# Kernel tuning notes

Measured on AMD Instinct MI355X. Metric: run time of the kernel, lower is better.

The kernel has to match this reference:

```python
import jax, jax.numpy as jnp
import numpy as np

B, HH, WW, DV, DC = 4, 128, 128, 768, 128
INNER = 2 * DV          # inner_ratio * values_dim = 1536
NH = 8                  # num_heads
DH = INNER // NH        # 192
SPACING = 4
COORDS_WEIGHT = 1.0     # attention_coords_weight
EPS = 1e-6


def _anchor_idx(h, w, s, shifted=False):
    rows = np.arange(0, h, s)
    cols = np.arange(0, w, s)
    if not shifted:
        rows = rows + ((h - 1) % s) // 2
        cols = cols + ((w - 1) % s) // 2
    return rows, cols


def _rms(x, w):
    return x * jax.lax.rsqrt(jnp.mean(x * x, axis=-1, keepdims=True) + EPS) * w


def _heads(x):  # (b, n, h*d) -> (b, h, n, d)
    b, n, _ = x.shape
    return x.reshape(b, n, NH, DH).transpose(0, 2, 1, 3)


def setup_inputs() -> dict:
    key = jax.random.key(0)
    ks = jax.random.split(key, 12)
    inp = {
        "values0": jax.random.normal(ks[0], (B, HH, WW, DV), jnp.float32),
        "coords0": jax.random.normal(ks[1], (B, HH, WW, DC), jnp.float32),
        "values1": jax.random.normal(ks[2], (B, HH, WW, DV), jnp.float32),
        "coords1": jax.random.normal(ks[3], (B, HH, WW, DC), jnp.float32),
        # values_to_qkv: Linear(DV, 3*INNER, bias=False), stored as (in, out)
        "w_qkv": jax.random.normal(ks[4], (DV, 3 * INNER), jnp.float32) * (DV ** -0.5),
        "qnorm_w": jnp.ones((INNER,), jnp.float32),
        "knorm_w": jnp.ones((INNER,), jnp.float32),
        # coords_to_qk: Linear(DC, 2*INNER, bias=False) + RMSNorm(2*INNER)
        "w_coords": jax.random.normal(ks[5], (DC, 2 * INNER), jnp.float32) * (DC ** -0.5),
        "coords_norm_w": jnp.ones((2 * INNER,), jnp.float32),
        "rel_pos_weight": jax.random.normal(ks[6], (1,), jnp.float32),
        # output_proj: Linear(INNER, DV)
        "out_w": jax.random.normal(ks[7], (INNER, DV), jnp.float32) * (INNER ** -0.5),
        "out_b": jnp.zeros((DV,), jnp.float32),
    }
    return inp


def reference(values0, coords0, values1, coords1, w_qkv, qnorm_w, knorm_w,
              w_coords, coords_norm_w, rel_pos_weight, out_w, out_b):
    rows, cols = _anchor_idx(HH, WW, SPACING)
    na = len(rows) * len(cols)  # anchors per source (1024)

    def gather(x):  # (B, HH, WW, D) -> (B, na, D)
        return x[:, rows[:, None], cols].reshape(B, na, -1)

    av = jnp.concatenate([gather(values0), gather(values1)], axis=1)  # (B, 2na, DV)
    ac = jnp.concatenate([gather(coords0), gather(coords1)], axis=1)  # (B, 2na, DC)

    qv, kv, vv = jnp.split(av @ w_qkv, 3, axis=-1)
    qv = _rms(qv, qnorm_w)
    kv = _rms(kv, knorm_w)
    qc, kc = jnp.split(_rms(ac @ w_coords, coords_norm_w), 2, axis=-1)

    qv, kv, vv, qc, kc = map(_heads, (qv, kv, vv, qc, kc))  # (B, NH, N, DH)

    scale = DH ** -0.5
    dots = jnp.einsum('bhqd,bhkd->bhqk', qv, kv) * scale
    rel = jnp.einsum('bhqd,bhkd->bhqk', qc, kc) * scale
    dots = dots + (rel_pos_weight[0] * COORDS_WEIGHT) * rel
    attn = jax.nn.softmax(dots, axis=-1)

    out = jnp.einsum('bhqk,bhkd->bhqd', attn, vv)          # (B, NH, N, DH)
    out = out.transpose(0, 2, 1, 3).reshape(B, 2 * na, INNER)
    out = out @ out_w + out_b                               # (B, 2na, DV)

    a0 = out[:, :na].reshape(B, len(rows), len(cols), DV)
    a1 = out[:, na:].reshape(B, len(rows), len(cols), DV)

    o0 = values0.at[:, rows[:, None], cols, :].add(a0)
    o1 = values1.at[:, rows[:, None], cols, :].add(a1)
    return jnp.stack([o0, o1])  # (2, B, HH, WW, DV)
```

## Files before the change

kernel.cpp:

```cpp
#include <hip/hip_runtime.h>

typedef unsigned short u16;
typedef unsigned int u32;
typedef float f32x4 __attribute__((ext_vector_type(4)));
typedef short bfx8 __attribute__((ext_vector_type(8)));
typedef u16 u16x8 __attribute__((ext_vector_type(8)));
typedef u16 u16x4 __attribute__((ext_vector_type(4)));

#define MFMA_BF16(a,b,c) __builtin_amdgcn_mfma_f32_16x16x32_bf16((a),(b),(c),0,0,0)
#define GL16(src, dst) __builtin_amdgcn_global_load_lds( \
    (const __attribute__((address_space(1))) u32*)(src), \
    (__attribute__((address_space(3))) u32*)(dst), 16, 0, 0)

__device__ __forceinline__ u16 f2bf(float f) {
  unsigned u = __float_as_uint(f);
  u += 0x7fffu + ((u >> 16) & 1u);
  return (u16)(u >> 16);
}
__device__ __forceinline__ float bf2f(u16 h) {
  return __uint_as_float((unsigned)h << 16);
}

#define SCALE_ATTN 0.07216878364870323f

__global__ __launch_bounds__(256) void wtrans_kernel(
    const float* __restrict__ in, u16* __restrict__ out, int K, int N)
{
  __shared__ float tile[32][33];
  int n0 = blockIdx.x * 32, k0 = blockIdx.y * 32;
  int tx = threadIdx.x, ty = threadIdx.y;
#pragma unroll
  for (int j = 0; j < 32; j += 8)
    tile[ty + j][tx] = in[(size_t)(k0 + ty + j) * N + n0 + tx];
  __syncthreads();
#pragma unroll
  for (int j = 0; j < 32; j += 8)
    out[(size_t)(n0 + ty + j) * K + k0 + tx] = f2bf(tile[tx][ty + j]);
}

__global__ __launch_bounds__(256) void gather_kernel(
    const float* __restrict__ v0, const float* __restrict__ c0,
    const float* __restrict__ v1, const float* __restrict__ c1,
    u16* __restrict__ av, u16* __restrict__ ac)
{
  int t = blockIdx.x;
  int b = t >> 11, n = t & 2047, s = n >> 10, a = n & 1023, rr = a >> 5, cc = a & 31;
  size_t pix = ((size_t)b * 128 + (1 + 4 * rr)) * 128 + (1 + 4 * cc);
  const float4* vs = (const float4*)((s ? v1 : v0) + pix * 768);
  const float4* cs = (const float4*)((s ? c1 : c0) + pix * 128);
  int tid = threadIdx.x;
  if (tid < 192) {
    float4 f = vs[tid];
    u16x4 o = { f2bf(f.x), f2bf(f.y), f2bf(f.z), f2bf(f.w) };
    *(u16x4*)(av + (size_t)t * 768 + tid * 4) = o;
  }
  if (tid < 32) {
    float4 f = cs[tid];
    u16x4 o = { f2bf(f.x), f2bf(f.y), f2bf(f.z), f2bf(f.w) };
    *(u16x4*)(ac + (size_t)t * 128 + tid * 4) = o;
  }
}

template<int EPILOG>
__global__ __launch_bounds__(256) void gemm128(
    const u16* __restrict__ A, const u16* __restrict__ Bt,
    int K, int lda, int ldb,
    u16* __restrict__ qp, u16* __restrict__ kp, u16* __restrict__ vT,
    float* __restrict__ outAdd, const float* __restrict__ bias)
{
  __shared__ u16 As[128 * 32];
  __shared__ u16 Bs[128 * 32];
  const int tid = threadIdx.x;
  const int wid = tid >> 6, lane = tid & 63;
  const int g = lane >> 4, q15 = lane & 15;
  const int wm = wid >> 1, wn = wid & 1;
  const int m0 = blockIdx.y * 128, n0 = blockIdx.x * 128;

  const u16* ga = A + (size_t)(m0 + (tid >> 2)) * lda + (tid & 3) * 8;
  const u16* gb = Bt + (size_t)(n0 + (tid >> 2)) * ldb + (tid & 3) * 8;
  u16* lA0 = &As[tid * 8]; u16* lA1 = &As[2048 + tid * 8];
  u16* lB0 = &Bs[tid * 8]; u16* lB1 = &Bs[2048 + tid * 8];
  const size_t a64 = (size_t)64 * lda, b64 = (size_t)64 * ldb;

  const f32x4 zero = {0.f, 0.f, 0.f, 0.f};
  f32x4 acc[4][4];
#pragma unroll
  for (int i = 0; i < 4; i++)
#pragma unroll
    for (int j = 0; j < 4; j++) acc[i][j] = zero;

  for (int kk = 0; kk < K; kk += 32) {
    GL16(ga + kk, lA0);
    GL16(ga + kk + a64, lA1);
    GL16(gb + kk, lB0);
    GL16(gb + kk + b64, lB1);
    __syncthreads();
    bfx8 af[4], bf[4];
#pragma unroll
    for (int mt = 0; mt < 4; mt++)
      af[mt] = *(const bfx8*)&As[(wm * 64 + mt * 16 + q15) * 32 + g * 8];
#pragma unroll
    for (int nt = 0; nt < 4; nt++)
      bf[nt] = *(const bfx8*)&Bs[(wn * 64 + nt * 16 + q15) * 32 + g * 8];
#pragma unroll
    for (int mt = 0; mt < 4; mt++)
#pragma unroll
      for (int nt = 0; nt < 4; nt++)
        acc[mt][nt] = MFMA_BF16(af[mt], bf[nt], acc[mt][nt]);
    __syncthreads();
  }

#pragma unroll
  for (int mt = 0; mt < 4; mt++) {
#pragma unroll
    for (int nt = 0; nt < 4; nt++) {
      const int tt = m0 + wm * 64 + mt * 16 + g * 4;
      const int c = n0 + wn * 64 + nt * 16 + q15;
      f32x4 v = acc[mt][nt];
      if (EPILOG == 0) {
        int isK = c >= 1536;
        int ck = isK ? c - 1536 : c;
        int hh = ck / 192, dd = ck - hh * 192;
#pragma unroll
        for (int j = 0; j < 4; j++) {
          int t = tt + j, b = t >> 11, n = t & 2047;
          size_t ro = ((size_t)(b * 8 + hh) * 2048 + n) * 384;
          u16 val = f2bf(v[j]);
          if (!isK) qp[ro + 192 + dd] = val;
          else      kp[ro + (size_t)((((24 + (dd >> 3)) ^ (n & 7)) << 3) + (dd & 7))] = val;
        }
      } else if (EPILOG == 1) {
        float bb = bias[c];
#pragma unroll
        for (int j = 0; j < 4; j++) {
          int t = tt + j, b = t >> 11, n = t & 2047;
          int s = n >> 10, a = n & 1023, rr = a >> 5, cc2 = a & 31;
          size_t orow = (size_t)(s * 4 + b) * 16384 + (size_t)(1 + 4 * rr) * 128 + (1 + 4 * cc2);
          outAdd[orow * 768 + c] += v[j] + bb;
        }
      } else {
        if (c < 1536) {
          int hh = c / 192, dd = c - hh * 192;
#pragma unroll
          for (int j = 0; j < 4; j++) {
            int t = tt + j, b = t >> 11, n = t & 2047;
            size_t ro = ((size_t)(b * 8 + hh) * 2048 + n) * 384;
            qp[ro + dd] = f2bf(v[j]);
          }
        } else if (c < 3072) {
          int ck = c - 1536;
          int hh = ck / 192, dd = ck - hh * 192;
          int chunk = dd >> 3, e = dd & 7;
#pragma unroll
          for (int j = 0; j < 4; j++) {
            int t = tt + j, b = t >> 11, n = t & 2047;
            size_t ro = ((size_t)(b * 8 + hh) * 2048 + n) * 384;
            kp[ro + (size_t)(((chunk ^ (n & 7)) << 3) + e)] = f2bf(v[j]);
          }
        } else {
          int cv = c - 3072;
          int hh = cv / 192, dv = cv - hh * 192;
          int t0 = tt, b = t0 >> 11, n = t0 & 2047;
          u16x4 o = { f2bf(v[0]), f2bf(v[1]), f2bf(v[2]), f2bf(v[3]) };
          *(u16x4*)(vT + ((size_t)(b * 8 + hh) * 192 + dv) * 2048 + n) = o;
        }
      }
    }
  }
}

__global__ __launch_bounds__(192) void rms_all_kernel(
    u16* __restrict__ qpack, u16* __restrict__ kpack,
    const float* __restrict__ qnw, const float* __restrict__ knw,
    const float* __restrict__ cnw, const float* __restrict__ relw)
{
  __shared__ float red[3][3];
  int t = blockIdx.x, tid = threadIdx.x;
  int b = t >> 11, n = t & 2047;
  float sqv = 0.f, skv = 0.f, sc = 0.f;
  u16x8 uqv, ukv, uqc, ukc;
  int h = tid / 24, c = tid % 24;
  size_t ro = ((size_t)(b * 8 + h) * 2048 + n) * 384;
  uqv = *(const u16x8*)(qpack + ro + c * 8);
  ukv = *(const u16x8*)(kpack + ro + ((c ^ (n & 7)) * 8));
  uqc = *(const u16x8*)(qpack + ro + 192 + c * 8);
  ukc = *(const u16x8*)(kpack + ro + (((24 + c) ^ (n & 7)) * 8));
#pragma unroll
  for (int e = 0; e < 8; e++) {
    float a = bf2f(uqv[e]); sqv += a * a;
    float d = bf2f(ukv[e]); skv += d * d;
    float x = bf2f(uqc[e]); sc += x * x;
    float y = bf2f(ukc[e]); sc += y * y;
  }
#pragma unroll
  for (int o = 32; o >= 1; o >>= 1) {
    sqv += __shfl_xor(sqv, o); skv += __shfl_xor(skv, o); sc += __shfl_xor(sc, o);
  }
  int wv = tid >> 6;
  if ((tid & 63) == 0) { red[0][wv] = sqv; red[1][wv] = skv; red[2][wv] = sc; }
  __syncthreads();
  sqv = red[0][0] + red[0][1] + red[0][2];
  skv = red[1][0] + red[1][1] + red[1][2];
  sc  = red[2][0] + red[2][1] + red[2][2];
  float fqv = rsqrtf(sqv * (1.f / 1536.f) + 1e-6f) * SCALE_ATTN;
  float fkv = rsqrtf(skv * (1.f / 1536.f) + 1e-6f);
  float fc  = rsqrtf(sc * (1.f / 3072.f) + 1e-6f);
  float fqc = fc * SCALE_ATTN * relw[0];
  u16x8 o0, o1, o2, o3;
#pragma unroll
  for (int e = 0; e < 8; e++) {
    int col = tid * 8 + e;
    o0[e] = f2bf(bf2f(uqv[e]) * fqv * qnw[col]);
    o1[e] = f2bf(bf2f(ukv[e]) * fkv * knw[col]);
    o2[e] = f2bf(bf2f(uqc[e]) * fqc * cnw[col]);
    o3[e] = f2bf(bf2f(ukc[e]) * fc  * cnw[1536 + col]);
  }
  *(u16x8*)(qpack + ro + c * 8) = o0;
  *(u16x8*)(kpack + ro + ((c ^ (n & 7)) * 8)) = o1;
  *(u16x8*)(qpack + ro + 192 + c * 8) = o2;
  *(u16x8*)(kpack + ro + (((24 + c) ^ (n & 7)) * 8)) = o3;
}

__global__ __launch_bounds__(256, 2) void attn_kernel(
    const u16* __restrict__ qpack, const u16* __restrict__ kpack,
    const u16* __restrict__ vT, u16* __restrict__ attnO,
    const float* __restrict__ cpy_v0, const float* __restrict__ cpy_v1,
    float* __restrict__ cpy_out)
{
  __shared__ u16 Ks[2][32 * 384];
  __shared__ u16 Vs[2][192 * 32];

  const int tid = threadIdx.x;
  const int wid = tid >> 6, lane = tid & 63;
  const int g = lane >> 4, q15 = lane & 15;
  const int bid = blockIdx.x;
  const int bh = (bid & 7) * 4 + ((bid >> 3) >> 4);
  const int q0 = ((bid >> 3) & 15) * 128 + wid * 32;
  const int b = bh >> 3, h = bh & 7;
  const int sw = q15 & 7;
  const int vsw = g ^ (q15 & 3);
  const bool hi = g >= 2;
  const int srcA = q15 + ((g & 1) << 5);

  const f32x4* cs0 = (const f32x4*)cpy_v0;
  const f32x4* cs1 = (const f32x4*)cpy_v1;
  f32x4* cdst = (f32x4*)cpy_out;
  const size_t cgid = (size_t)bid * 256 + tid;
  const size_t CHALF = 12582912ull;
  const size_t CSLAB = 8388608ull;

  bfx8 qf[2][12];
  {
    const u16* qb = qpack + ((size_t)bh * 2048 + q0 + q15) * 384 + g * 8;
#pragma unroll
    for (int s = 0; s < 2; s++)
#pragma unroll
      for (int c = 0; c < 12; c++)
        qf[s][c] = *(const bfx8*)(qb + s * 16 * 384 + c * 32);
  }

  const f32x4 zero = {0.f, 0.f, 0.f, 0.f};
  f32x4 acc[2][12];
#pragma unroll
  for (int s = 0; s < 2; s++)
#pragma unroll
    for (int i = 0; i < 12; i++) acc[s][i] = zero;
  float m0 = -3e30f, m1 = -3e30f, l0 = 0.f, l1 = 0.f;

  const char* kg = (const char*)(kpack + (size_t)bh * 2048 * 384);
  const char* vg = (const char*)(vT + (size_t)bh * 192 * 2048);

  auto stage = [&](int buf, int kb) {
    const char* ks = kg + (size_t)kb * 768;
#pragma unroll
    for (int j = 0; j < 6; j++) {
      int off = j * 4096 + tid * 16;
      GL16(ks + off, (char*)&Ks[buf][0] + off);
    }
    const char* vsrc = vg + (size_t)kb * 2;
#pragma unroll
    for (int j = 0; j < 3; j++) {
      int off = j * 4096 + tid * 16;
      int row = off >> 6;
      int cc = (tid & 3) ^ (row & 3);
      GL16(vsrc + (size_t)row * 4096 + cc * 16, (char*)&Vs[buf][0] + off);
    }
  };

  stage(0, 0);
  asm volatile("s_waitcnt vmcnt(0)" ::: "memory");
  __builtin_amdgcn_s_barrier();

  int cur = 0;
  f32x4 cr0, cr1, cr2;
  for (int t = 0; t < 64; t++) {
    if (t > 0) {
      const size_t pb = (size_t)(t - 1) * 131072ull + cgid;
      __builtin_nontemporal_store(cr0, &cdst[pb]);
      __builtin_nontemporal_store(cr1, &cdst[pb + CSLAB]);
      __builtin_nontemporal_store(cr2, &cdst[pb + 2 * CSLAB]);
    }
    if (t < 63) stage(cur ^ 1, (t + 1) * 32);
    {
      const size_t i0 = (size_t)t * 131072ull + cgid;
      const size_t i1 = i0 + CSLAB, i2 = i0 + 2 * CSLAB;
      cr0 = __builtin_nontemporal_load(&cs0[i0]);
      cr1 = (i1 < CHALF) ? __builtin_nontemporal_load(&cs0[i1])
                         : __builtin_nontemporal_load(&cs1[i1 - CHALF]);
      cr2 = __builtin_nontemporal_load(&cs1[i2 - CHALF]);
    }

    f32x4 s00 = zero, s01 = zero, s10 = zero, s11 = zero;
    const u16* Kc = &Ks[cur][0];
    __builtin_amdgcn_s_setprio(1);
#pragma unroll
    for (int c = 0; c < 12; c++) {
      int ch = ((((c << 2) + g) ^ sw) << 3);
      bfx8 k0 = *(const bfx8*)(Kc + q15 * 384 + ch);
      bfx8 k1 = *(const bfx8*)(Kc + (q15 + 16) * 384 + ch);
      s00 = MFMA_BF16(k0, qf[0][c], s00);
      s01 = MFMA_BF16(k0, qf[1][c], s01);
      s10 = MFMA_BF16(k1, qf[0][c], s10);
      s11 = MFMA_BF16(k1, qf[1][c], s11);
    }
    __builtin_amdgcn_s_setprio(0);

    float bm0 = fmaxf(fmaxf(fmaxf(s00[0], s00[1]), fmaxf(s00[2], s00[3])),
                      fmaxf(fmaxf(s10[0], s10[1]), fmaxf(s10[2], s10[3])));
    float bm1 = fmaxf(fmaxf(fmaxf(s01[0], s01[1]), fmaxf(s01[2], s01[3])),
                      fmaxf(fmaxf(s11[0], s11[1]), fmaxf(s11[2], s11[3])));

    if (__any((bm0 > m0 + 8.f) | (bm1 > m1 + 8.f))) {
      bm0 = fmaxf(bm0, __shfl_xor(bm0, 16)); bm0 = fmaxf(bm0, __shfl_xor(bm0, 32));
      bm1 = fmaxf(bm1, __shfl_xor(bm1, 16)); bm1 = fmaxf(bm1, __shfl_xor(bm1, 32));
      float n0 = fmaxf(m0, bm0), n1 = fmaxf(m1, bm1);
      float c0 = __expf(m0 - n0), c1 = __expf(m1 - n1);
      l0 *= c0; l1 *= c1;
#pragma unroll
      for (int i = 0; i < 12; i++) {
#pragma unroll
        for (int j = 0; j < 4; j++) { acc[0][i][j] *= c0; acc[1][i][j] *= c1; }
      }
      m0 = n0; m1 = n1;
    }

    float p0[8], p1[8];
    float rs0 = 0.f, rs1 = 0.f;
#pragma unroll
    for (int j = 0; j < 4; j++) {
      p0[j]     = __expf(s00[j] - m0);
      p0[4 + j] = __expf(s10[j] - m0);
      p1[j]     = __expf(s01[j] - m1);
      p1[4 + j] = __expf(s11[j] - m1);
      rs0 += p0[j] + p0[4 + j];
      rs1 += p1[j] + p1[4 + j];
    }
    l0 += rs0; l1 += rs1;

    union { bfx8 v; u32 w[4]; } pt0, pt1;
    {
      u32 w0 = (u32)f2bf(p0[0]) | ((u32)f2bf(p0[1]) << 16);
      u32 w1 = (u32)f2bf(p0[2]) | ((u32)f2bf(p0[3]) << 16);
      u32 w2 = (u32)f2bf(p0[4]) | ((u32)f2bf(p0[5]) << 16);
      u32 w3 = (u32)f2bf(p0[6]) | ((u32)f2bf(p0[7]) << 16);
      u32 a0 = __shfl((int)w0, srcA),      b0 = __shfl((int)w2, srcA);
      u32 a1 = __shfl((int)w1, srcA),      b1 = __shfl((int)w3, srcA);
      u32 a2 = __shfl((int)w0, srcA + 16), b2 = __shfl((int)w2, srcA + 16);
      u32 a3 = __shfl((int)w1, srcA + 16), b3 = __shfl((int)w3, srcA + 16);
      pt0.w[0] = hi ? b0 : a0; pt0.w[1] = hi ? b1 : a1;
      pt0.w[2] = hi ? b2 : a2; pt0.w[3] = hi ? b3 : a3;
    }
    {
      u32 w0 = (u32)f2bf(p1[0]) | ((u32)f2bf(p1[1]) << 16);
      u32 w1 = (u32)f2bf(p1[2]) | ((u32)f2bf(p1[3]) << 16);
      u32 w2 = (u32)f2bf(p1[4]) | ((u32)f2bf(p1[5]) << 16);
      u32 w3 = (u32)f2bf(p1[6]) | ((u32)f2bf(p1[7]) << 16);
      u32 a0 = __shfl((int)w0, srcA),      b0 = __shfl((int)w2, srcA);
      u32 a1 = __shfl((int)w1, srcA),      b1 = __shfl((int)w3, srcA);
      u32 a2 = __shfl((int)w0, srcA + 16), b2 = __shfl((int)w2, srcA + 16);
      u32 a3 = __shfl((int)w1, srcA + 16), b3 = __shfl((int)w3, srcA + 16);
      pt1.w[0] = hi ? b0 : a0; pt1.w[1] = hi ? b1 : a1;
      pt1.w[2] = hi ? b2 : a2; pt1.w[3] = hi ? b3 : a3;
    }

    const u16* Vc = &Vs[cur][0];
    __builtin_amdgcn_s_setprio(1);
#pragma unroll
    for (int dt = 0; dt < 12; dt++) {
      bfx8 vf = *(const bfx8*)(Vc + dt * 512 + q15 * 32 + vsw * 8);
      acc[0][dt] = MFMA_BF16(vf, pt0.v, acc[0][dt]);
      acc[1][dt] = MFMA_BF16(vf, pt1.v, acc[1][dt]);
    }
    __builtin_amdgcn_s_setprio(0);

    asm volatile("s_waitcnt vmcnt(3)" ::: "memory");
    __builtin_amdgcn_s_barrier();
    cur ^= 1;
  }

  {
    const size_t pb = (size_t)63 * 131072ull + cgid;
    __builtin_nontemporal_store(cr0, &cdst[pb]);
    __builtin_nontemporal_store(cr1, &cdst[pb + CSLAB]);
    __builtin_nontemporal_store(cr2, &cdst[pb + 2 * CSLAB]);
  }

  l0 += __shfl_xor(l0, 16); l0 += __shfl_xor(l0, 32);
  l1 += __shfl_xor(l1, 16); l1 += __shfl_xor(l1, 32);

  float li0 = 1.f / l0, li1 = 1.f / l1;
  u16* ob = attnO + ((size_t)(b * 2048 + q0 + q15)) * 1536 + h * 192;
#pragma unroll
  for (int dt = 0; dt < 12; dt++) {
    u16x4 o0, o1;
#pragma unroll
    for (int j = 0; j < 4; j++) {
      o0[j] = f2bf(acc[0][dt][j] * li0);
      o1[j] = f2bf(acc[1][dt][j] * li1);
    }
    *(u16x4*)(ob + dt * 16 + g * 4) = o0;
    *(u16x4*)(ob + (size_t)16 * 1536 + dt * 16 + g * 4) = o1;
  }
}

extern "C" void kernel_launch(void* const* d_in, const int* in_sizes, int n_in,
                              void* d_out, int out_size, void* d_ws, size_t ws_size,
                              hipStream_t stream)
{
  const float* values0 = (const float*)d_in[0];
  const float* coords0 = (const float*)d_in[1];
  const float* values1 = (const float*)d_in[2];
  const float* coords1 = (const float*)d_in[3];
  const float* w_qkv   = (const float*)d_in[4];
  const float* qnorm_w = (const float*)d_in[5];
  const float* knorm_w = (const float*)d_in[6];
  const float* w_coords= (const float*)d_in[7];
  const float* cnorm_w = (const float*)d_in[8];
  const float* relw    = (const float*)d_in[9];
  const float* out_w   = (const float*)d_in[10];
  const float* out_b   = (const float*)d_in[11];
  float* out = (float*)d_out;
  (void)in_sizes; (void)n_in; (void)out_size; (void)ws_size;

  char* ws = (char*)d_ws;
  u16* qpack   = (u16*)(ws);
  u16* kpack   = (u16*)(ws + 50331648ull);
  u16* vT      = (u16*)(ws + 100663296ull);
  u16* attnO   = (u16*)(ws + 125829120ull);
  u16* av      = (u16*)(ws + 150994944ull);
  u16* ac      = (u16*)(ws + 163577856ull);
  u16* wqkvT   = (u16*)(ws + 165675008ull);
  u16* wcoordT = (u16*)(ws + 172752896ull);
  u16* outwT   = (u16*)(ws + 173539328ull);

  wtrans_kernel<<<dim3(144, 24), dim3(32, 8), 0, stream>>>(w_qkv, wqkvT, 768, 4608);
  wtrans_kernel<<<dim3(96, 4),   dim3(32, 8), 0, stream>>>(w_coords, wcoordT, 128, 3072);
  wtrans_kernel<<<dim3(24, 48),  dim3(32, 8), 0, stream>>>(out_w, outwT, 1536, 768);
  gather_kernel<<<8192, 256, 0, stream>>>(values0, coords0, values1, coords1, av, ac);

  gemm128<2><<<dim3(36, 64), 256, 0, stream>>>(av, wqkvT, 768, 768, 768,
                                               qpack, kpack, vT, nullptr, nullptr);
  gemm128<0><<<dim3(24, 64), 256, 0, stream>>>(ac, wcoordT, 128, 128, 128,
                                               qpack, kpack, nullptr, nullptr, nullptr);

  rms_all_kernel<<<8192, 192, 0, stream>>>(qpack, kpack, qnorm_w, knorm_w, cnorm_w, relw);

  attn_kernel<<<512, 256, 0, stream>>>(qpack, kpack, vT, attnO,
                                       values0, values1, out);

  gemm128<1><<<dim3(6, 64), 256, 0, stream>>>(attnO, outwT, 1536, 1536, 1536,
                                              nullptr, nullptr, nullptr, out, out_b);
}
```

Baseline: 493.1 us.

## Split output projection into 64-row GEMM and reorder attention prefetch stores

Replaces the 128x128-tile output-projection GEMM (384 blocks) with a dedicated 64x128-tile kernel launched on 768 blocks, so more workgroups fill the GPU for this small GEMM. The new kernel is a simple single-buffered loop with two barriers per K step, so it gives up overlap of loads with compute. In the attention kernel, the K/V staging for the next tile is now issued before the nontemporal copy stores, and the wait count is relaxed to account for the stores now in flight. The intent is to start the next tile's loads earlier.

```diff
diff --git a/kernel.cpp b/kernel.cpp
--- a/kernel.cpp
+++ b/kernel.cpp
@@ -128,15 +128,6 @@
           u16 val = f2bf(v[j]);
           if (!isK) qp[ro + 192 + dd] = val;
           else      kp[ro + (size_t)((((24 + (dd >> 3)) ^ (n & 7)) << 3) + (dd & 7))] = val;
-        }
-      } else if (EPILOG == 1) {
-        float bb = bias[c];
-#pragma unroll
-        for (int j = 0; j < 4; j++) {
-          int t = tt + j, b = t >> 11, n = t & 2047;
-          int s = n >> 10, a = n & 1023, rr = a >> 5, cc2 = a & 31;
-          size_t orow = (size_t)(s * 4 + b) * 16384 + (size_t)(1 + 4 * rr) * 128 + (1 + 4 * cc2);
-          outAdd[orow * 768 + c] += v[j] + bb;
         }
       } else {
         if (c < 1536) {
@@ -169,6 +160,71 @@
   }
 }
 
+__global__ __launch_bounds__(256) void gemm_out64(
+    const u16* __restrict__ A, const u16* __restrict__ Bt,
+    float* __restrict__ outAdd, const float* __restrict__ bias)
+{
+  __shared__ u16 As[64 * 32];
+  __shared__ u16 Bs[128 * 32];
+  const int K = 1536;
+  const int tid = threadIdx.x;
+  const int wid = tid >> 6, lane = tid & 63;
+  const int g = lane >> 4, q15 = lane & 15;
+  const int wm = wid >> 1, wn = wid & 1;
+  const int m0 = blockIdx.y * 64, n0 = blockIdx.x * 128;
+
+  const u16* ga = A + (size_t)(m0 + (tid >> 2)) * K + (tid & 3) * 8;
+  const u16* gb = Bt + (size_t)(n0 + (tid >> 2)) * K + (tid & 3) * 8;
+  u16* lA0 = &As[tid * 8];
+  u16* lB0 = &Bs[tid * 8]; u16* lB1 = &Bs[2048 + tid * 8];
+  const size_t b64 = (size_t)64 * K;
+
+  const f32x4 zero = {0.f, 0.f, 0.f, 0.f};
+  f32x4 acc[2][4];
+#pragma unroll
+  for (int i = 0; i < 2; i++)
+#pragma unroll
+    for (int j = 0; j < 4; j++) acc[i][j] = zero;
+
+  for (int kk = 0; kk < K; kk += 32) {
+    GL16(ga + kk, lA0);
+    GL16(gb + kk, lB0);
+    GL16(gb + kk + b64, lB1);
+    __syncthreads();
+    bfx8 af[2], bf[4];
+#pragma unroll
+    for (int mt = 0; mt < 2; mt++)
+      af[mt] = *(const bfx8*)&As[(wm * 32 + mt * 16 + q15) * 32 + g * 8];
+#pragma unroll
+    for (int nt = 0; nt < 4; nt++)
+      bf[nt] = *(const bfx8*)&Bs[(wn * 64 + nt * 16 + q15) * 32 + g * 8];
+#pragma unroll
+    for (int mt = 0; mt < 2; mt++)
+#pragma unroll
+      for (int nt = 0; nt < 4; nt++)
+        acc[mt][nt] = MFMA_BF16(af[mt], bf[nt], acc[mt][nt]);
+    __syncthreads();
+  }
+
+#pragma unroll
+  for (int mt = 0; mt < 2; mt++) {
+#pragma unroll
+    for (int nt = 0; nt < 4; nt++) {
+      const int tt = m0 + wm * 32 + mt * 16 + g * 4;
+      const int c = n0 + wn * 64 + nt * 16 + q15;
+      f32x4 v = acc[mt][nt];
+      float bb = bias[c];
+#pragma unroll
+      for (int j = 0; j < 4; j++) {
+        int t = tt + j, b = t >> 11, n = t & 2047;
+        int s = n >> 10, a = n & 1023, rr = a >> 5, cc2 = a & 31;
+        size_t orow = (size_t)(s * 4 + b) * 16384 + (size_t)(1 + 4 * rr) * 128 + (1 + 4 * cc2);
+        outAdd[orow * 768 + c] += v[j] + bb;
+      }
+    }
+  }
+}
+
 __global__ __launch_bounds__(192) void rms_all_kernel(
     u16* __restrict__ qpack, u16* __restrict__ kpack,
     const float* __restrict__ qnw, const float* __restrict__ knw,
@@ -294,13 +350,15 @@
   int cur = 0;
   f32x4 cr0, cr1, cr2;
   for (int t = 0; t < 64; t++) {
+    if (t < 63) stage(cur ^ 1, (t + 1) * 32);
+    asm volatile("" ::: "memory");
     if (t > 0) {
       const size_t pb = (size_t)(t - 1) * 131072ull + cgid;
       __builtin_nontemporal_store(cr0, &cdst[pb]);
       __builtin_nontemporal_store(cr1, &cdst[pb + CSLAB]);
       __builtin_nontemporal_store(cr2, &cdst[pb + 2 * CSLAB]);
     }
-    if (t < 63) stage(cur ^ 1, (t + 1) * 32);
+    asm volatile("" ::: "memory");
     {
       const size_t i0 = (size_t)t * 131072ull + cgid;
       const size_t i1 = i0 + CSLAB, i2 = i0 + 2 * CSLAB;
@@ -393,7 +451,8 @@
     }
     __builtin_amdgcn_s_setprio(0);
 
-    asm volatile("s_waitcnt vmcnt(3)" ::: "memory");
+    if (t == 0) asm volatile("s_waitcnt vmcnt(3)" ::: "memory");
+    else        asm volatile("s_waitcnt vmcnt(6)" ::: "memory");
     __builtin_amdgcn_s_barrier();
     cur ^= 1;
   }
@@ -468,6 +527,5 @@
   attn_kernel<<<512, 256, 0, stream>>>(qpack, kpack, vT, attnO,
                                        values0, values1, out);
 
-  gemm128<1><<<dim3(6, 64), 256, 0, stream>>>(attnO, outwT, 1536, 1536, 1536,
-                                              nullptr, nullptr, nullptr, out, out_b);
-}
+  gemm_out64<<<dim3(6, 128), 256, 0, stream>>>(attnO, outwT, out, out_b);
+}
```

After: 521.4 us. +5.8%, slower.
